# Kernel tuning notes

Measured on AMD Instinct MI355X. Metric: run time of the kernel, lower is better.

Reference implementation:

```python
import jax, jax.numpy as jnp
import numpy as np

R = 3.9
EPS = 0.3
BETA = 0.15
STEPS = 15


def setup_inputs() -> dict:
    key = jax.random.key(0)
    k1, k2 = jax.random.split(key)
    drive = jax.random.uniform(k1, (2048, 1, 16384), dtype=jnp.float32)
    K = jnp.abs(jax.random.uniform(k2, (3,), dtype=jnp.float32))
    K = K / K.sum()
    return {"drive": drive, "K": K}


def reference(drive, K):
    # Circular 3-tap conv: torch conv1d is cross-correlation, padded circularly,
    # so local[i] = K[0]*m[i-1] + K[1]*m[i] + K[2]*m[i+1] (indices mod L).
    def step(grid, _):
        mapped = R * grid * (1.0 - grid)
        local = (K[0] * jnp.roll(mapped, 1, axis=-1)
                 + K[1] * mapped
                 + K[2] * jnp.roll(mapped, -1, axis=-1))
        physics = (1.0 - EPS) * mapped + EPS * local
        grid = (1.0 - BETA) * physics + BETA * drive
        return grid, None

    grid, _ = jax.lax.scan(step, drive, None, length=STEPS)
    return jnp.clip(grid, 0.0001, 1.0 - 0.0001)
```

## Files before the change

### kernel.cpp

```cpp
#include <hip/hip_runtime.h>
#include <stdint.h>


constexpr float Rc    = 3.9f;
constexpr float EPSc  = 0.3f;
constexpr float BETAc = 0.15f;
constexpr int   STEPS = 15;
constexpr int   L     = 16384;
constexpr int   CE    = 9;
constexpr int   HALF  = 4;
constexpr int   NP    = HALF + 1;
constexpr int   SEG   = 512;
constexpr int   GHOST = 32;
constexpr int   EXT   = SEG + 2*GHOST;
constexpr int   TPB   = 256;
constexpr int   WPB   = TPB / 64;
constexpr int   SPR   = L / SEG;

constexpr int DPP_WAVE_SHL1 = 0x130;
constexpr int DPP_WAVE_SHR1 = 0x138;

__device__ __forceinline__ float dpp_shr1(float x) {
    return __int_as_float(__builtin_amdgcn_update_dpp(
        0, __float_as_int(x), DPP_WAVE_SHR1, 0xf, 0xf, true));
}
__device__ __forceinline__ float dpp_shl1(float x) {
    return __int_as_float(__builtin_amdgcn_update_dpp(
        0, __float_as_int(x), DPP_WAVE_SHL1, 0xf, 0xf, true));
}

__device__ __forceinline__ float2 pk_mul(float2 a, float2 b) {
    float2 d;
    asm("v_pk_mul_f32 %0, %1, %2" : "=v"(d) : "v"(a), "v"(b));
    return d;
}
__device__ __forceinline__ float2 pk_fma(float2 a, float2 b, float2 c) {
    float2 d;
    asm("v_pk_fma_f32 %0, %1, %2, %3" : "=v"(d) : "v"(a), "v"(b), "v"(c));
    return d;
}
__device__ __forceinline__ float2 pk_fma_na(float2 a, float2 b, float2 c) {
    float2 d;
    asm("v_pk_fma_f32 %0, %1, %2, %3 neg_lo:[1,0,0] neg_hi:[1,0,0]"
        : "=v"(d) : "v"(a), "v"(b), "v"(c));
    return d;
}

typedef const __attribute__((address_space(1))) float gfloat;
typedef __attribute__((address_space(3))) float lfloat;

__global__ __launch_bounds__(TPB, 8)
void cml1d_kernel(const float* __restrict__ drive,
                  const float* __restrict__ K,
                  float* __restrict__ out) {
    __shared__ float lds[WPB][EXT];

    const int lane = threadIdx.x & 63;
    const int wv   = threadIdx.x >> 6;
    const int gw   = blockIdx.x * WPB + wv;
    const int row  = gw >> 5;
    const int seg  = gw & (SPR - 1);
    const float* base = drive + (size_t)row * L;
    const int wb = seg * SEG - GHOST;

    float* buf = &lds[wv][0];
    #pragma unroll
    for (int j = 0; j < 2; ++j) {
        int idx = (wb + j * 256 + lane * 4) & (L - 1);
        __builtin_amdgcn_global_load_lds((gfloat*)(base + idx),
                                         (lfloat*)(buf + j * 256), 16, 0, 0);
    }
    {
        int idx = (wb + 512 + lane) & (L - 1);
        __builtin_amdgcn_global_load_lds((gfloat*)(base + idx),
                                         (lfloat*)(buf + 512), 4, 0, 0);
    }

    const float K0 = K[0], K1 = K[1], K2 = K[2];
    const float A  = (1.0f - BETAc) * (1.0f - EPSc);
    const float B  = (1.0f - BETAc) * EPSc;
    const float d0 = Rc * (B * K0);
    const float d1 = Rc * (A + B * K1);
    const float d2 = Rc * (B * K2);
    const float2 D0 = make_float2(d0, d0);
    const float2 D1 = make_float2(d1, d1);
    const float2 D2 = make_float2(d2, d2);
    const float2 B2 = make_float2(BETAc, BETAc);

    asm volatile("s_waitcnt vmcnt(0)" ::: "memory");

    float2 P[NP], BD[NP];
    #pragma unroll
    for (int j = 0; j < NP; ++j) {
        P[j]  = make_float2(buf[lane * CE + j], buf[lane * CE + j + HALF]);
        BD[j] = pk_mul(B2, P[j]);
    }

    for (int s = 0; s < STEPS; ++s) {
        float2 MH[NP];
        #pragma unroll
        for (int j = 0; j < NP; ++j)
            MH[j] = pk_fma_na(P[j], P[j], P[j]);

        const float mleft  = dpp_shr1(MH[NP - 1].y);
        const float mright = dpp_shl1(MH[0].x);
        const float2 MHm1_0 = make_float2(mleft, MH[HALF - 1].x);
        const float2 MHp1_T = make_float2(MH[1].y, mright);

        #pragma unroll
        for (int j = 0; j < NP; ++j) {
            float2 a = (j == 0)      ? MHm1_0 : MH[j - 1];
            float2 b = (j == NP - 1) ? MHp1_T : MH[j + 1];
            P[j] = pk_fma(D0, a, pk_fma(D1, MH[j], pk_fma(D2, b, BD[j])));
        }
    }

    __builtin_amdgcn_wave_barrier();
    #pragma unroll
    for (int j = 0; j < NP; ++j) {
        buf[lane * CE + j]        = P[j].x;
        buf[lane * CE + j + HALF] = P[j].y;
    }
    __builtin_amdgcn_wave_barrier();

    const float lo = 0.0001f;
    const float hi = 0.9999f;
    float* op = out + (size_t)row * L + seg * SEG;
    #pragma unroll
    for (int j = 0; j < 2; ++j) {
        int f = j * 64 + lane;
        float4 v = *reinterpret_cast<float4*>(&buf[GHOST + f * 4]);
        v.x = __builtin_amdgcn_fmed3f(v.x, lo, hi);
        v.y = __builtin_amdgcn_fmed3f(v.y, lo, hi);
        v.z = __builtin_amdgcn_fmed3f(v.z, lo, hi);
        v.w = __builtin_amdgcn_fmed3f(v.w, lo, hi);
        *reinterpret_cast<float4*>(op + f * 4) = v;
    }
}

extern "C" void kernel_launch(void* const* d_in, const int* in_sizes, int n_in,
                              void* d_out, int out_size, void* d_ws, size_t ws_size,
                              hipStream_t stream) {
    const float* drive = (const float*)d_in[0];
    const float* K     = (const float*)d_in[1];
    float* out         = (float*)d_out;
    const int rows   = in_sizes[0] / L;
    const int blocks = rows * SPR / WPB;
    cml1d_kernel<<<dim3(blocks), dim3(TPB), 0, stream>>>(drive, K, out);
}
```

Baseline: 232.7 us.

## Make kernel persistent with double-buffered LDS prefetch of next segment

Switches to a fixed grid of 2048 blocks where each wave processes eight segments in turn, prefetching the next segment into a second LDS buffer with global_load_lds while it computes the current one. This is meant to hide global load latency behind the 15-step stencil compute and to cut per-block launch overhead. In exchange it doubles LDS per block, which may lower occupancy. It also hardcodes the grid size and row count, so it only covers the full input when rows*SPR/WPB equals NBLK*T, and it relies on a partial vmcnt wait ordering.

```diff
diff --git a/kernel.cpp b/kernel.cpp
--- a/kernel.cpp
+++ b/kernel.cpp
@@ -16,6 +16,8 @@
 constexpr int   TPB   = 256;
 constexpr int   WPB   = TPB / 64;
 constexpr int   SPR   = L / SEG;
+constexpr int   NBLK  = 2048;
+constexpr int   T     = 8;
 
 constexpr int DPP_WAVE_SHL1 = 0x130;
 constexpr int DPP_WAVE_SHR1 = 0x138;
@@ -53,28 +55,11 @@
 void cml1d_kernel(const float* __restrict__ drive,
                   const float* __restrict__ K,
                   float* __restrict__ out) {
-    __shared__ float lds[WPB][EXT];
+    __shared__ float lds[WPB][2][EXT];
 
     const int lane = threadIdx.x & 63;
     const int wv   = threadIdx.x >> 6;
-    const int gw   = blockIdx.x * WPB + wv;
-    const int row  = gw >> 5;
-    const int seg  = gw & (SPR - 1);
-    const float* base = drive + (size_t)row * L;
-    const int wb = seg * SEG - GHOST;
-
-    float* buf = &lds[wv][0];
-    #pragma unroll
-    for (int j = 0; j < 2; ++j) {
-        int idx = (wb + j * 256 + lane * 4) & (L - 1);
-        __builtin_amdgcn_global_load_lds((gfloat*)(base + idx),
-                                         (lfloat*)(buf + j * 256), 16, 0, 0);
-    }
-    {
-        int idx = (wb + 512 + lane) & (L - 1);
-        __builtin_amdgcn_global_load_lds((gfloat*)(base + idx),
-                                         (lfloat*)(buf + 512), 4, 0, 0);
-    }
+    const int gw0  = blockIdx.x * WPB + wv;
 
     const float K0 = K[0], K1 = K[1], K2 = K[2];
     const float A  = (1.0f - BETAc) * (1.0f - EPSc);
@@ -87,54 +72,91 @@
     const float2 D2 = make_float2(d2, d2);
     const float2 B2 = make_float2(BETAc, BETAc);
 
-    asm volatile("s_waitcnt vmcnt(0)" ::: "memory");
+    auto prefetch = [&](int gw, float* buf) {
+        const int row = gw >> 5, seg = gw & (SPR - 1);
+        const float* base = drive + (size_t)row * L;
+        const int wb = seg * SEG - GHOST;
+        #pragma unroll
+        for (int j = 0; j < 2; ++j) {
+            int idx = (wb + j * 256 + lane * 4) & (L - 1);
+            __builtin_amdgcn_global_load_lds((gfloat*)(base + idx),
+                                             (lfloat*)(buf + j * 256), 16, 0, 0);
+        }
+        int idx = (wb + 512 + lane) & (L - 1);
+        __builtin_amdgcn_global_load_lds((gfloat*)(base + idx),
+                                         (lfloat*)(buf + 512), 4, 0, 0);
+    };
 
     float2 P[NP], BD[NP];
-    #pragma unroll
-    for (int j = 0; j < NP; ++j) {
-        P[j]  = make_float2(buf[lane * CE + j], buf[lane * CE + j + HALF]);
-        BD[j] = pk_mul(B2, P[j]);
-    }
-
-    for (int s = 0; s < STEPS; ++s) {
-        float2 MH[NP];
-        #pragma unroll
-        for (int j = 0; j < NP; ++j)
-            MH[j] = pk_fma_na(P[j], P[j], P[j]);
-
-        const float mleft  = dpp_shr1(MH[NP - 1].y);
-        const float mright = dpp_shl1(MH[0].x);
-        const float2 MHm1_0 = make_float2(mleft, MH[HALF - 1].x);
-        const float2 MHp1_T = make_float2(MH[1].y, mright);
-
+    auto unpack = [&](const float* buf) {
         #pragma unroll
         for (int j = 0; j < NP; ++j) {
-            float2 a = (j == 0)      ? MHm1_0 : MH[j - 1];
-            float2 b = (j == NP - 1) ? MHp1_T : MH[j + 1];
-            P[j] = pk_fma(D0, a, pk_fma(D1, MH[j], pk_fma(D2, b, BD[j])));
+            P[j]  = make_float2(buf[lane * CE + j], buf[lane * CE + j + HALF]);
+            BD[j] = pk_mul(B2, P[j]);
+            asm volatile("" : "+v"(P[j]), "+v"(BD[j]));
         }
-    }
+    };
 
-    __builtin_amdgcn_wave_barrier();
-    #pragma unroll
-    for (int j = 0; j < NP; ++j) {
-        buf[lane * CE + j]        = P[j].x;
-        buf[lane * CE + j + HALF] = P[j].y;
-    }
-    __builtin_amdgcn_wave_barrier();
+    prefetch(gw0, &lds[wv][0][0]);
+    asm volatile("s_waitcnt vmcnt(0)" ::: "memory");
+    unpack(&lds[wv][0][0]);
 
-    const float lo = 0.0001f;
-    const float hi = 0.9999f;
-    float* op = out + (size_t)row * L + seg * SEG;
-    #pragma unroll
-    for (int j = 0; j < 2; ++j) {
-        int f = j * 64 + lane;
-        float4 v = *reinterpret_cast<float4*>(&buf[GHOST + f * 4]);
-        v.x = __builtin_amdgcn_fmed3f(v.x, lo, hi);
-        v.y = __builtin_amdgcn_fmed3f(v.y, lo, hi);
-        v.z = __builtin_amdgcn_fmed3f(v.z, lo, hi);
-        v.w = __builtin_amdgcn_fmed3f(v.w, lo, hi);
-        *reinterpret_cast<float4*>(op + f * 4) = v;
+    int cur = 0;
+    #pragma unroll 1
+    for (int t = 0; t < T; ++t) {
+        if (t < T - 1)
+            prefetch((t + 1) * (NBLK * WPB) + gw0, &lds[wv][cur ^ 1][0]);
+        __builtin_amdgcn_sched_barrier(0);
+
+        for (int s = 0; s < STEPS; ++s) {
+            float2 MH[NP];
+            #pragma unroll
+            for (int j = 0; j < NP; ++j)
+                MH[j] = pk_fma_na(P[j], P[j], P[j]);
+
+            const float mleft  = dpp_shr1(MH[NP - 1].y);
+            const float mright = dpp_shl1(MH[0].x);
+            const float2 MHm1_0 = make_float2(mleft, MH[HALF - 1].x);
+            const float2 MHp1_T = make_float2(MH[1].y, mright);
+
+            #pragma unroll
+            for (int j = 0; j < NP; ++j) {
+                float2 a = (j == 0)      ? MHm1_0 : MH[j - 1];
+                float2 b = (j == NP - 1) ? MHp1_T : MH[j + 1];
+                P[j] = pk_fma(D0, a, pk_fma(D1, MH[j], pk_fma(D2, b, BD[j])));
+            }
+        }
+
+        const int gw  = t * (NBLK * WPB) + gw0;
+        const int row = gw >> 5, seg = gw & (SPR - 1);
+        float* tb = &lds[wv][cur][0];
+        __builtin_amdgcn_wave_barrier();
+        #pragma unroll
+        for (int j = 0; j < NP; ++j) {
+            tb[lane * CE + j]        = P[j].x;
+            tb[lane * CE + j + HALF] = P[j].y;
+        }
+        __builtin_amdgcn_wave_barrier();
+
+        const float lo = 0.0001f;
+        const float hi = 0.9999f;
+        float* op = out + (size_t)row * L + seg * SEG;
+        #pragma unroll
+        for (int j = 0; j < 2; ++j) {
+            int f = j * 64 + lane;
+            float4 v = *reinterpret_cast<float4*>(&tb[GHOST + f * 4]);
+            v.x = __builtin_amdgcn_fmed3f(v.x, lo, hi);
+            v.y = __builtin_amdgcn_fmed3f(v.y, lo, hi);
+            v.z = __builtin_amdgcn_fmed3f(v.z, lo, hi);
+            v.w = __builtin_amdgcn_fmed3f(v.w, lo, hi);
+            *reinterpret_cast<float4*>(op + f * 4) = v;
+        }
+
+        if (t < T - 1) {
+            asm volatile("s_waitcnt vmcnt(2)" ::: "memory");
+            unpack(&lds[wv][cur ^ 1][0]);
+            cur ^= 1;
+        }
     }
 }
 
@@ -144,7 +166,5 @@
     const float* drive = (const float*)d_in[0];
     const float* K     = (const float*)d_in[1];
     float* out         = (float*)d_out;
-    const int rows   = in_sizes[0] / L;
-    const int blocks = rows * SPR / WPB;
-    cml1d_kernel<<<dim3(blocks), dim3(TPB), 0, stream>>>(drive, K, out);
+    cml1d_kernel<<<dim3(NBLK), dim3(TPB), 0, stream>>>(drive, K, out);
 }
```

After: 234.6 us. Within noise of the previous version (+0.8%).
